# Performance work log

Measured on AMD Instinct MI355X. Metric: run time of the kernel, lower is better.

## Reference

```python
import jax, jax.numpy as jnp
import numpy as np

N = 50000
E = 800000
DIN = 128
DOUT = 128
T = 4  # number of edge types: onset, consecutive, during, rest


def setup_inputs() -> dict:
    key = jax.random.key(0)
    ks = jax.random.split(key, 12)
    s = 1.0 / np.sqrt(DIN)
    inp = {
        "x": jax.random.normal(ks[0], (N, DIN), dtype=jnp.float32),
        "edge_index": jax.random.randint(ks[1], (2, E), 0, N, dtype=jnp.int32),
        "edge_type": jax.random.randint(ks[2], (E,), 0, T, dtype=jnp.int32),
        # stacked per-etype parameters of ResGatedGraphConv
        "Wk": jax.random.uniform(ks[3], (T, DIN, DOUT), jnp.float32, -s, s),
        "bk": jax.random.uniform(ks[4], (T, DOUT), jnp.float32, -s, s),
        "Wq": jax.random.uniform(ks[5], (T, DIN, DOUT), jnp.float32, -s, s),
        "bq": jax.random.uniform(ks[6], (T, DOUT), jnp.float32, -s, s),
        "Wv": jax.random.uniform(ks[7], (T, DIN, DOUT), jnp.float32, -s, s),
        "bv": jax.random.uniform(ks[8], (T, DOUT), jnp.float32, -s, s),
        "Ws": jax.random.uniform(ks[9], (T, DIN, DOUT), jnp.float32, -s, s),
        "b": jax.random.uniform(ks[10], (T, DOUT), jnp.float32, -s, s),
    }
    return inp


def reference(x, edge_index, edge_type, Wk, bk, Wq, bq, Wv, bv, Ws, b):
    # PyG ResGatedGraphConv per edge type t, with edges masked to that type:
    #   out_i = sum_{j->i, type==t} sigmoid(k_i + q_j) * v_j + Ws_t x_i + b_t
    # followed by mean over edge types ('mean' reduction).
    src = edge_index[0]  # j (message source)
    dst = edge_index[1]  # i (message target)
    n = x.shape[0]
    outs = []
    for t in range(T):
        k = x @ Wk[t] + bk[t]  # [N, DOUT]
        q = x @ Wq[t] + bq[t]
        v = x @ Wv[t] + bv[t]
        eta = jax.nn.sigmoid(k[dst] + q[src])        # [E, DOUT]
        msg = eta * v[src]                            # [E, DOUT]
        msg = jnp.where((edge_type == t)[:, None], msg, 0.0)
        agg = jax.ops.segment_sum(msg, dst, num_segments=n)
        outs.append(agg + x @ Ws[t] + b[t])
    return jnp.mean(jnp.stack(outs, axis=0), axis=0)  # [N, DOUT]
```

## Files before the change

kernel.cpp:

```cpp
#include <hip/hip_runtime.h>

typedef unsigned short u16;
typedef unsigned int u32;
typedef __attribute__((ext_vector_type(8))) short bf16x8;
typedef __attribute__((ext_vector_type(4))) float f32x4;
typedef __attribute__((ext_vector_type(4))) u16 u16x4;
typedef __attribute__((ext_vector_type(2))) u32 u32x2;

#define DIM 128
#define ROWB 2304
#define QV_SPAN 384
#define K_OFF 1536
#define S_OFF 2048
#define AS1C(p) ((const __attribute__((address_space(1))) void*)(p))
#define AS3P(p) ((__attribute__((address_space(3))) void*)(p))

#define QKSCALE -1.44269504088896341f

#if defined(__has_builtin)
#if __has_builtin(__builtin_amdgcn_exp2f)
#define EXP2(x) __builtin_amdgcn_exp2f(x)
#endif
#endif
#ifndef EXP2
extern "C" __device__ float __ocml_exp2_f32(float);
#define EXP2(x) __ocml_exp2_f32(x)
#endif

__device__ __forceinline__ u32 f2bf(float f){
  u32 x = __float_as_uint(f);
  return (x + 0x7fffu + ((x >> 16) & 1u)) >> 16;
}
__device__ __forceinline__ float bf2f(u16 u){
  return __uint_as_float(((u32)u) << 16);
}

__global__ __launch_bounds__(256) void prep_kernel(
    const float* __restrict__ x, u16* __restrict__ xb,
    const int* __restrict__ dst, int* __restrict__ cnt, int* __restrict__ rank,
    const float* __restrict__ Wk, const float* __restrict__ bk,
    const float* __restrict__ Wq, const float* __restrict__ bq,
    const float* __restrict__ Wv, const float* __restrict__ bv,
    const float* __restrict__ Ws, const float* __restrict__ bb,
    u16* __restrict__ WcatT, float* __restrict__ biascat,
    int T, int N, int E, int rows){
  int id = blockIdx.x * 256 + threadIdx.x;
  if (id < E){
    rank[id] = atomicAdd(&cnt[dst[id]], 1);
    return;
  }
  id -= E;
  int total_w = (3 * T + 1) * DIM * DIM;
  if (id < total_w){
    int kk = id & (DIM - 1);
    int c  = id >> 7;
    int nt = c >> 7;
    int j  = c & (DIM - 1);
    float wv, bvv;
    if (nt < T)        { wv = Wq[(nt*DIM + kk)*DIM + j] * QKSCALE;       bvv = bq[nt*DIM + j] * QKSCALE; }
    else if (nt < 2*T) { wv = Wv[((nt-T)*DIM + kk)*DIM + j];             bvv = bv[(nt-T)*DIM + j]; }
    else if (nt < 3*T) { wv = Wk[((nt-2*T)*DIM + kk)*DIM + j] * QKSCALE; bvv = bk[(nt-2*T)*DIM + j] * QKSCALE; }
    else {
      float s = 0.f, sb = 0.f;
      for (int t = 0; t < T; ++t){ s += Ws[(t*DIM + kk)*DIM + j]; sb += bb[t*DIM + j]; }
      wv = s / (float)T; bvv = sb / (float)T;
    }
    WcatT[(size_t)c * DIM + kk] = (u16)f2bf(wv);
    if (kk == 0) biascat[c] = bvv;
    return;
  }
  id -= total_w;
  int total_cast = rows * (DIM / 4);
  if (id < total_cast){
    int el = id * 4;
    int node = el >> 7;
    u32x2 pk;
    if (node < N){
      f32x4 v = *(const f32x4*)(x + el);
      pk.x = f2bf(v.x) | (f2bf(v.y) << 16);
      pk.y = f2bf(v.z) | (f2bf(v.w) << 16);
    } else { pk.x = 0u; pk.y = 0u; }
    *(u32x2*)(xb + el) = pk;
  }
}

__global__ __launch_bounds__(256) void scan1_kernel(const int* __restrict__ cnt,
                                                    int* __restrict__ offs,
                                                    int* __restrict__ bsum, int n){
  __shared__ int wsum[4];
  const int tid = threadIdx.x;
  const int lane = tid & 63, wave = tid >> 6;
  const int base = blockIdx.x * 2048 + tid * 8;
  int v[8]; int tot = 0;
#pragma unroll
  for (int j = 0; j < 8; ++j){
    int idx = base + j;
    int val = (idx < n) ? cnt[idx] : 0;
    v[j] = val; tot += val;
  }
  int incl = tot;
#pragma unroll
  for (int d = 1; d < 64; d <<= 1){
    int u = __shfl_up(incl, d, 64);
    if (lane >= d) incl += u;
  }
  if (lane == 63) wsum[wave] = incl;
  __syncthreads();
  int wbase = 0;
#pragma unroll
  for (int w = 0; w < 4; ++w) if (w < wave) wbase += wsum[w];
  int excl = wbase + incl - tot;
  if (tid == 255) bsum[blockIdx.x] = wbase + incl;
#pragma unroll
  for (int j = 0; j < 8; ++j){
    int idx = base + j;
    if (idx < n) offs[idx] = excl;
    excl += v[j];
  }
}

__global__ __launch_bounds__(64) void scan2_kernel(const int* __restrict__ bsum,
                                                   int* __restrict__ boffs, int nb){
  int lane = threadIdx.x;
  int v = (lane < nb) ? bsum[lane] : 0;
  int incl = v;
#pragma unroll
  for (int d = 1; d < 64; d <<= 1){
    int u = __shfl_up(incl, d, 64);
    if (lane >= d) incl += u;
  }
  if (lane < nb) boffs[lane] = incl - v;
}

__global__ __launch_bounds__(256, 4) void gemm_scatter_kernel(
    const u16* __restrict__ xb, const u16* __restrict__ WcatT,
    const float* __restrict__ biascat, char* __restrict__ Y,
    const int* __restrict__ src, const int* __restrict__ dst,
    const int* __restrict__ et, const int* __restrict__ offs,
    const int* __restrict__ boffs, const int* __restrict__ rank,
    int* __restrict__ packed,
    int N, int E, int T, int NB, int mtiles, int nsc){
  __shared__ u16 wt[DIM * DIM];
  int bid = blockIdx.x;
  if (bid < nsc){
    int e = bid * 256 + threadIdx.x;
    if (e < E){
      int d = dst[e];
      int pos = offs[d] + boffs[d >> 11] + rank[e];
      int t = et[e] & 3;
      packed[pos] = src[e] * ROWB + t * QV_SPAN + (t << 28);
    }
    return;
  }
  bid -= nsc;
  int body = NB * (mtiles & ~7);
  int mt, nt;
  if (bid < body){
    int g = bid >> 3, r = bid & 7;
    int a = g / NB;
    mt = a * 8 + r;
    nt = g - a * NB;
  } else {
    int z = bid - body;
    mt = (mtiles & ~7) + z / NB;
    nt = z % NB;
  }
  const int m0 = mt * 128;
  const int n0 = nt * 128;
  const int tid  = threadIdx.x;
  const int wave = tid >> 6;
  const int lane = tid & 63;
  const int l15  = lane & 15;
  const int quad = lane >> 4;
  const int wrow = wave * 32;

  const u16* xrow0 = xb + (size_t)(m0 + wrow + l15) * DIM + quad * 8;
  const u16* xrow1 = xrow0 + 16 * DIM;

  bf16x8 bfr[2][4];
#pragma unroll
  for (int ks = 0; ks < 4; ++ks){
    bfr[0][ks] = *(const bf16x8*)(xrow0 + ks * 32);
    bfr[1][ks] = *(const bf16x8*)(xrow1 + ks * 32);
  }

#pragma unroll
  for (int it = 0; it < 8; ++it){
    int s  = it * 256 + tid;
    int r  = s >> 4;
    int p  = s & 15;
    int lb = p ^ (r & 7);
    int lbase = (it * 256 + wave * 64) * 8;
    __builtin_amdgcn_global_load_lds(AS1C(WcatT + (size_t)(n0 + r) * DIM + lb * 8),
                                     AS3P(wt + lbase), 16, 0, 0);
  }
  __syncthreads();

  f32x4 acc[2][8];
#pragma unroll
  for (int m = 0; m < 2; ++m)
#pragma unroll
    for (int f = 0; f < 8; ++f)
      acc[m][f] = (f32x4){0.f, 0.f, 0.f, 0.f};

#pragma unroll
  for (int ks = 0; ks < 4; ++ks){
    const int pb8 = (((ks * 4 + quad) ^ (l15 & 7)) * 8);
#pragma unroll
    for (int f = 0; f < 8; ++f){
      bf16x8 afr = *(const bf16x8*)&wt[(f * 16 + l15) * DIM + pb8];
      acc[0][f] = __builtin_amdgcn_mfma_f32_16x16x32_bf16(afr, bfr[0][ks], acc[0][f], 0, 0, 0);
      acc[1][f] = __builtin_amdgcn_mfma_f32_16x16x32_bf16(afr, bfr[1][ks], acc[1][f], 0, 0, 0);
    }
  }

  __syncthreads();
  char* lds = (char*)wt;
  const bool is_q = (nt < T);
  const bool is_k = (nt >= 2*T) && (nt < 3*T);
  if (is_q || is_k){
    const int boffb = is_q ? (nt * QV_SPAN) : (K_OFF + (nt - 2*T) * 128);
#pragma unroll
    for (int m = 0; m < 2; ++m){
      const int nl = wrow + m * 16 + l15;
#pragma unroll
      for (int f = 0; f < 8; ++f){
        const int feat = f * 16 + quad * 4;
        f32x4 b4 = *(const f32x4*)&biascat[n0 + feat];
        f32x4 v  = acc[m][f];
        u32 w = __builtin_amdgcn_cvt_pk_fp8_f32(v.x + b4.x, v.y + b4.y, 0, false);
        w = __builtin_amdgcn_cvt_pk_fp8_f32(v.z + b4.z, v.w + b4.w, w, true);
        *(u32*)(lds + nl * 128 + (feat ^ ((nl & 7) << 4))) = w;
      }
    }
    __syncthreads();
    const int seg = tid & 7;
    const int nr0 = tid >> 3;
#pragma unroll
    for (int pass = 0; pass < 4; ++pass){
      const int nl = pass * 32 + nr0;
      f32x4 d = *(const f32x4*)(lds + nl * 128 + ((seg ^ (nl & 7)) << 4));
      *(f32x4*)(Y + (size_t)(m0 + nl) * ROWB + boffb + seg * 16) = d;
    }
  } else {
    const int boffb = (nt < 2*T) ? ((nt - T) * QV_SPAN + 128) : S_OFF;
#pragma unroll
    for (int m = 0; m < 2; ++m){
      const int nl = wrow + m * 16 + l15;
#pragma unroll
      for (int f = 0; f < 8; ++f){
        const int feat = f * 16 + quad * 4;
        f32x4 b4 = *(const f32x4*)&biascat[n0 + feat];
        f32x4 v  = acc[m][f];
        u32 lo = f2bf(v.x + b4.x) | (f2bf(v.y + b4.y) << 16);
        u32 hi = f2bf(v.z + b4.z) | (f2bf(v.w + b4.w) << 16);
        u32x2 pk = {lo, hi};
        *(u32x2*)(lds + nl * 256 + ((feat * 2) ^ ((nl & 7) << 4))) = pk;
      }
    }
    __syncthreads();
    const int seg = tid & 15;
    const int nr0 = tid >> 4;
#pragma unroll
    for (int pass = 0; pass < 8; ++pass){
      const int nl = pass * 16 + nr0;
      f32x4 d = *(const f32x4*)(lds + nl * 256 + ((seg ^ (nl & 7)) << 4));
      *(f32x4*)(Y + (size_t)(m0 + nl) * ROWB + boffb + seg * 16) = d;
    }
  }
}

__global__ __launch_bounds__(256) void agg_kernel(const char* __restrict__ Y,
                                                  const int* __restrict__ offs,
                                                  const int* __restrict__ boffs,
                                                  const int* __restrict__ packed,
                                                  float* __restrict__ out,
                                                  int N, int E, float invT){
  __shared__ float klds[8 * 512];
  const int wave = threadIdx.x >> 6;
  const int lane = threadIdx.x & 63;
  const int half = lane >> 5;
  const int l32  = lane & 31;
  const int hh   = wave * 2 + half;
  const int node = blockIdx.x * 8 + hh;
  const bool valid = node < N;
  const int nc = valid ? node : N - 1;

  const char* yr = Y + (size_t)nc * ROWB;
  char* kb = (char*)(klds + hh * 512 + l32 * 4);

#pragma unroll
  for (int t = 0; t < 4; ++t){
    u32 kw = *(const u32*)(yr + K_OFF + t * 128 + l32 * 4);
    f32x4 kt = (f32x4){ __builtin_amdgcn_cvt_f32_fp8(kw, 0), __builtin_amdgcn_cvt_f32_fp8(kw, 1),
                        __builtin_amdgcn_cvt_f32_fp8(kw, 2), __builtin_amdgcn_cvt_f32_fp8(kw, 3) };
    *(f32x4*)(kb + t * 512) = kt;
  }
  u16x4 sw = *(const u16x4*)(yr + S_OFF + l32 * 8);

  int e0 = 0, e1 = 0;
  if (valid){
    e0 = offs[nc] + boffs[nc >> 11];
    e1 = (nc == N - 1) ? E : (offs[nc + 1] + boffs[(nc + 1) >> 11]);
  }

  const u32 qoff_l = (u32)(l32 * 4);
  const u32 voff_l = (u32)(128 + l32 * 8);

  f32x4 acc = {0.f, 0.f, 0.f, 0.f};
  int e = e0;
  for (; e + 8 <= e1; e += 8){
    int p[8];
#pragma unroll
    for (int j = 0; j < 8; ++j) p[j] = packed[e + j];
    u32 qw[8]; u16x4 vw[8]; f32x4 kt[8];
#pragma unroll
    for (int j = 0; j < 8; ++j){
      u32 base = (u32)p[j] & 0x07FFFFFFu;
      qw[j] = *(const u32*)(Y + base + qoff_l);
      vw[j] = *(const u16x4*)(Y + base + voff_l);
      kt[j] = *(const f32x4*)(kb + (((u32)p[j] >> 19) & 0x600u));
    }
#pragma unroll
    for (int j = 0; j < 8; ++j){
      acc.x += bf2f(vw[j].x) * __builtin_amdgcn_rcpf(1.f + EXP2(kt[j].x + __builtin_amdgcn_cvt_f32_fp8(qw[j], 0)));
      acc.y += bf2f(vw[j].y) * __builtin_amdgcn_rcpf(1.f + EXP2(kt[j].y + __builtin_amdgcn_cvt_f32_fp8(qw[j], 1)));
      acc.z += bf2f(vw[j].z) * __builtin_amdgcn_rcpf(1.f + EXP2(kt[j].z + __builtin_amdgcn_cvt_f32_fp8(qw[j], 2)));
      acc.w += bf2f(vw[j].w) * __builtin_amdgcn_rcpf(1.f + EXP2(kt[j].w + __builtin_amdgcn_cvt_f32_fp8(qw[j], 3)));
    }
  }
  for (; e < e1; ++e){
    int p = packed[e];
    u32 base = (u32)p & 0x07FFFFFFu;
    u32 qw = *(const u32*)(Y + base + qoff_l);
    u16x4 vw = *(const u16x4*)(Y + base + voff_l);
    f32x4 kt = *(const f32x4*)(kb + (((u32)p >> 19) & 0x600u));
    acc.x += bf2f(vw.x) * __builtin_amdgcn_rcpf(1.f + EXP2(kt.x + __builtin_amdgcn_cvt_f32_fp8(qw, 0)));
    acc.y += bf2f(vw.y) * __builtin_amdgcn_rcpf(1.f + EXP2(kt.y + __builtin_amdgcn_cvt_f32_fp8(qw, 1)));
    acc.z += bf2f(vw.z) * __builtin_amdgcn_rcpf(1.f + EXP2(kt.z + __builtin_amdgcn_cvt_f32_fp8(qw, 2)));
    acc.w += bf2f(vw.w) * __builtin_amdgcn_rcpf(1.f + EXP2(kt.w + __builtin_amdgcn_cvt_f32_fp8(qw, 3)));
  }
  if (valid){
    f32x4 o = { invT * acc.x + bf2f(sw.x), invT * acc.y + bf2f(sw.y),
                invT * acc.z + bf2f(sw.z), invT * acc.w + bf2f(sw.w) };
    *(f32x4*)&out[(size_t)node * DIM + l32 * 4] = o;
  }
}

extern "C" void kernel_launch(void* const* d_in, const int* in_sizes, int n_in,
                              void* d_out, int out_size, void* d_ws, size_t ws_size,
                              hipStream_t stream){
  const float* x  = (const float*)d_in[0];
  const int*   ei = (const int*)d_in[1];
  const int*   et = (const int*)d_in[2];
  const float* Wk = (const float*)d_in[3];
  const float* bk = (const float*)d_in[4];
  const float* Wq = (const float*)d_in[5];
  const float* bq = (const float*)d_in[6];
  const float* Wv = (const float*)d_in[7];
  const float* bv = (const float*)d_in[8];
  const float* Ws = (const float*)d_in[9];
  const float* bb = (const float*)d_in[10];
  float* out = (float*)d_out;

  const int N = in_sizes[0] / DIM;
  const int E = in_sizes[2];
  const int T = in_sizes[3] / (DIM * DIM);
  const int NB = 3 * T + 1;
  const int ncol = NB * DIM;
  const int mtiles = (N + 127) / 128;
  const int rows = mtiles * 128;
  const int nscan = (N + 2047) / 2048;
  const int nsc = (E + 255) / 256;

  char* ws = (char*)d_ws;
  size_t off = 0;
  auto alloc = [&](size_t bytes) -> char* {
    char* p = ws + off;
    off = (off + bytes + 255) & ~(size_t)255;
    return p;
  };
  u16*   xb      = (u16*)alloc((size_t)rows * DIM * 2);
  u16*   WcatT   = (u16*)alloc((size_t)ncol * DIM * 2);
  float* biascat = (float*)alloc((size_t)ncol * 4);
  char*  Y       = (char*)alloc((size_t)rows * ROWB);
  int*   cnt     = (int*)alloc((size_t)N * 4);
  int*   offs    = (int*)alloc((size_t)N * 4);
  int*   rank    = (int*)alloc((size_t)E * 4);
  int*   packed  = (int*)alloc((size_t)E * 4);
  int*   bsum    = (int*)alloc((size_t)nscan * 4);
  int*   boffs   = (int*)alloc((size_t)nscan * 4);
  (void)ws_size; (void)n_in; (void)out_size;

  const int* srcp = ei;
  const int* dstp = ei + E;

  hipMemsetAsync(cnt, 0, (size_t)N * 4, stream);
  int prep_total = E + NB * DIM * DIM + rows * (DIM / 4);
  prep_kernel<<<(prep_total + 255) / 256, 256, 0, stream>>>(
      x, xb, dstp, cnt, rank, Wk, bk, Wq, bq, Wv, bv, Ws, bb,
      WcatT, biascat, T, N, E, rows);
  scan1_kernel<<<nscan, 256, 0, stream>>>(cnt, offs, bsum, N);
  scan2_kernel<<<1, 64, 0, stream>>>(bsum, boffs, nscan);
  gemm_scatter_kernel<<<nsc + NB * mtiles, 256, 0, stream>>>(
      xb, WcatT, biascat, Y, srcp, dstp, et, offs, boffs, rank, packed,
      N, E, T, NB, mtiles, nsc);
  agg_kernel<<<(N + 7) / 8, 256, 0, stream>>>(Y, offs, boffs, packed, out, N, E, 1.0f / (float)T);
}
```

Measured before the change: 247.9 us.

## Software-pipeline edge index loads and replace scalar tail with masked rounds in aggregation

The aggregation loop now prefetches the next round's eight packed edge indices while gathering and computing the current round, so index latency overlaps with the Y gathers. The scalar remainder loop is replaced by clamped index loads, with out-of-range edges masked by zeroing their V values, so every node runs whole 8-edge rounds. Launch bounds now request 8 blocks per SM to limit register use. The cost is wasted gather and compute on padded edges for nodes with small degree, plus possible register spills under the tighter bound.

```diff
diff --git a/kernel.cpp b/kernel.cpp
--- a/kernel.cpp
+++ b/kernel.cpp
@@ -270,7 +270,7 @@
   }
 }
 
-__global__ __launch_bounds__(256) void agg_kernel(const char* __restrict__ Y,
+__global__ __launch_bounds__(256, 8) void agg_kernel(const char* __restrict__ Y,
                                                   const int* __restrict__ offs,
                                                   const int* __restrict__ boffs,
                                                   const int* __restrict__ packed,
@@ -289,6 +289,12 @@
   const char* yr = Y + (size_t)nc * ROWB;
   char* kb = (char*)(klds + hh * 512 + l32 * 4);
 
+  int e0 = 0, e1 = 0;
+  if (valid){
+    e0 = offs[nc] + boffs[nc >> 11];
+    e1 = (nc == N - 1) ? E : (offs[nc + 1] + boffs[(nc + 1) >> 11]);
+  }
+
 #pragma unroll
   for (int t = 0; t < 4; ++t){
     u32 kw = *(const u32*)(yr + K_OFF + t * 128 + l32 * 4);
@@ -298,47 +304,52 @@
   }
   u16x4 sw = *(const u16x4*)(yr + S_OFF + l32 * 8);
 
-  int e0 = 0, e1 = 0;
-  if (valid){
-    e0 = offs[nc] + boffs[nc >> 11];
-    e1 = (nc == N - 1) ? E : (offs[nc + 1] + boffs[(nc + 1) >> 11]);
-  }
-
   const u32 qoff_l = (u32)(l32 * 4);
   const u32 voff_l = (u32)(128 + l32 * 8);
 
+  const int nrounds = (e1 - e0 + 7) >> 3;
+  const int last = (e1 > e0) ? (e1 - 1) : 0;
+
   f32x4 acc = {0.f, 0.f, 0.f, 0.f};
+  int pcur[8];
+#pragma unroll
+  for (int j = 0; j < 8; ++j){
+    int idx = e0 + j; idx = idx > last ? last : idx;
+    pcur[j] = packed[idx];
+  }
   int e = e0;
-  for (; e + 8 <= e1; e += 8){
-    int p[8];
-#pragma unroll
-    for (int j = 0; j < 8; ++j) p[j] = packed[e + j];
-    u32 qw[8]; u16x4 vw[8]; f32x4 kt[8];
+  for (int r = 0; r < nrounds; ++r){
+    u32 qw[8]; u16x4 vw[8];
 #pragma unroll
     for (int j = 0; j < 8; ++j){
-      u32 base = (u32)p[j] & 0x07FFFFFFu;
+      u32 base = (u32)pcur[j] & 0x07FFFFFFu;
       qw[j] = *(const u32*)(Y + base + qoff_l);
       vw[j] = *(const u16x4*)(Y + base + voff_l);
-      kt[j] = *(const f32x4*)(kb + (((u32)p[j] >> 19) & 0x600u));
-    }
+    }
+    const int en = e + 8;
+    int pnext[8];
 #pragma unroll
     for (int j = 0; j < 8; ++j){
-      acc.x += bf2f(vw[j].x) * __builtin_amdgcn_rcpf(1.f + EXP2(kt[j].x + __builtin_amdgcn_cvt_f32_fp8(qw[j], 0)));
-      acc.y += bf2f(vw[j].y) * __builtin_amdgcn_rcpf(1.f + EXP2(kt[j].y + __builtin_amdgcn_cvt_f32_fp8(qw[j], 1)));
-      acc.z += bf2f(vw[j].z) * __builtin_amdgcn_rcpf(1.f + EXP2(kt[j].z + __builtin_amdgcn_cvt_f32_fp8(qw[j], 2)));
-      acc.w += bf2f(vw[j].w) * __builtin_amdgcn_rcpf(1.f + EXP2(kt[j].w + __builtin_amdgcn_cvt_f32_fp8(qw[j], 3)));
-    }
-  }
-  for (; e < e1; ++e){
-    int p = packed[e];
-    u32 base = (u32)p & 0x07FFFFFFu;
-    u32 qw = *(const u32*)(Y + base + qoff_l);
-    u16x4 vw = *(const u16x4*)(Y + base + voff_l);
-    f32x4 kt = *(const f32x4*)(kb + (((u32)p >> 19) & 0x600u));
-    acc.x += bf2f(vw.x) * __builtin_amdgcn_rcpf(1.f + EXP2(kt.x + __builtin_amdgcn_cvt_f32_fp8(qw, 0)));
-    acc.y += bf2f(vw.y) * __builtin_amdgcn_rcpf(1.f + EXP2(kt.y + __builtin_amdgcn_cvt_f32_fp8(qw, 1)));
-    acc.z += bf2f(vw.z) * __builtin_amdgcn_rcpf(1.f + EXP2(kt.z + __builtin_amdgcn_cvt_f32_fp8(qw, 2)));
-    acc.w += bf2f(vw.w) * __builtin_amdgcn_rcpf(1.f + EXP2(kt.w + __builtin_amdgcn_cvt_f32_fp8(qw, 3)));
+      int idx = en + j; idx = idx > last ? last : idx;
+      pnext[j] = packed[idx];
+    }
+#pragma unroll
+    for (int j = 0; j < 8; ++j){
+      f32x4 kt = *(const f32x4*)(kb + (((u32)pcur[j] >> 19) & 0x600u));
+      const bool live = (e + j) < e1;
+      u32x2 vv = *(u32x2*)&vw[j];
+      vv.x = live ? vv.x : 0u;
+      vv.y = live ? vv.y : 0u;
+      u16 v0 = (u16)(vv.x & 0xffffu), v1 = (u16)(vv.x >> 16);
+      u16 v2 = (u16)(vv.y & 0xffffu), v3 = (u16)(vv.y >> 16);
+      acc.x += bf2f(v0) * __builtin_amdgcn_rcpf(1.f + EXP2(kt.x + __builtin_amdgcn_cvt_f32_fp8(qw[j], 0)));
+      acc.y += bf2f(v1) * __builtin_amdgcn_rcpf(1.f + EXP2(kt.y + __builtin_amdgcn_cvt_f32_fp8(qw[j], 1)));
+      acc.z += bf2f(v2) * __builtin_amdgcn_rcpf(1.f + EXP2(kt.z + __builtin_amdgcn_cvt_f32_fp8(qw[j], 2)));
+      acc.w += bf2f(v3) * __builtin_amdgcn_rcpf(1.f + EXP2(kt.w + __builtin_amdgcn_cvt_f32_fp8(qw[j], 3)));
+    }
+#pragma unroll
+    for (int j = 0; j < 8; ++j) pcur[j] = pnext[j];
+    e = en;
   }
   if (valid){
     f32x4 o = { invT * acc.x + bf2f(sw.x), invT * acc.y + bf2f(sw.y),
```

Measured after the change: 304.2 us. 1.23x slower.

## Use one wave per node in aggregation with double-buffered edge gathers

Applied to the files above, without the earlier changes.

The aggregation kernel now assigns a full 64-lane wave to each destination node, with each lane handling 2 channels instead of 4, so there are twice as many waves. The edge loop is restructured into blocks of 6 edges with two register buffers, so the gathers for the next block are issued before the current block is computed, which is meant to hide gather latency. Out-of-range indices are clamped and their contributions masked, which adds some wasted loads on the tail. Gathers are narrower per lane, and the total work per node is spread across more threads.

```diff
diff --git a/kernel.cpp b/kernel.cpp
--- a/kernel.cpp
+++ b/kernel.cpp
@@ -4,6 +4,7 @@
 typedef unsigned int u32;
 typedef __attribute__((ext_vector_type(8))) short bf16x8;
 typedef __attribute__((ext_vector_type(4))) float f32x4;
+typedef __attribute__((ext_vector_type(2))) float f32x2;
 typedef __attribute__((ext_vector_type(4))) u16 u16x4;
 typedef __attribute__((ext_vector_type(2))) u32 u32x2;
 
@@ -276,74 +277,89 @@
                                                   const int* __restrict__ packed,
                                                   float* __restrict__ out,
                                                   int N, int E, float invT){
-  __shared__ float klds[8 * 512];
+  __shared__ float klds[4 * 4 * 128];
   const int wave = threadIdx.x >> 6;
   const int lane = threadIdx.x & 63;
-  const int half = lane >> 5;
-  const int l32  = lane & 31;
-  const int hh   = wave * 2 + half;
-  const int node = blockIdx.x * 8 + hh;
+  const int node = blockIdx.x * 4 + wave;
   const bool valid = node < N;
   const int nc = valid ? node : N - 1;
 
   const char* yr = Y + (size_t)nc * ROWB;
-  char* kb = (char*)(klds + hh * 512 + l32 * 4);
-
+
+  float* kwp = klds + wave * 512 + lane * 2;
 #pragma unroll
   for (int t = 0; t < 4; ++t){
-    u32 kw = *(const u32*)(yr + K_OFF + t * 128 + l32 * 4);
-    f32x4 kt = (f32x4){ __builtin_amdgcn_cvt_f32_fp8(kw, 0), __builtin_amdgcn_cvt_f32_fp8(kw, 1),
-                        __builtin_amdgcn_cvt_f32_fp8(kw, 2), __builtin_amdgcn_cvt_f32_fp8(kw, 3) };
-    *(f32x4*)(kb + t * 512) = kt;
-  }
-  u16x4 sw = *(const u16x4*)(yr + S_OFF + l32 * 8);
+    u32 kw = *(const u16*)(yr + K_OFF + t * 128 + lane * 2);
+    f32x2 kt2 = (f32x2){ __builtin_amdgcn_cvt_f32_fp8(kw, 0),
+                         __builtin_amdgcn_cvt_f32_fp8(kw, 1) };
+    *(f32x2*)(kwp + t * 128) = kt2;
+  }
+  u32 sw = *(const u32*)(yr + S_OFF + lane * 4);
 
   int e0 = 0, e1 = 0;
   if (valid){
     e0 = offs[nc] + boffs[nc >> 11];
     e1 = (nc == N - 1) ? E : (offs[nc + 1] + boffs[(nc + 1) >> 11]);
   }
-
-  const u32 qoff_l = (u32)(l32 * 4);
-  const u32 voff_l = (u32)(128 + l32 * 8);
-
-  f32x4 acc = {0.f, 0.f, 0.f, 0.f};
-  int e = e0;
-  for (; e + 8 <= e1; e += 8){
-    int p[8];
-#pragma unroll
-    for (int j = 0; j < 8; ++j) p[j] = packed[e + j];
-    u32 qw[8]; u16x4 vw[8]; f32x4 kt[8];
-#pragma unroll
-    for (int j = 0; j < 8; ++j){
-      u32 base = (u32)p[j] & 0x07FFFFFFu;
-      qw[j] = *(const u32*)(Y + base + qoff_l);
-      vw[j] = *(const u16x4*)(Y + base + voff_l);
-      kt[j] = *(const f32x4*)(kb + (((u32)p[j] >> 19) & 0x600u));
-    }
-#pragma unroll
-    for (int j = 0; j < 8; ++j){
-      acc.x += bf2f(vw[j].x) * __builtin_amdgcn_rcpf(1.f + EXP2(kt[j].x + __builtin_amdgcn_cvt_f32_fp8(qw[j], 0)));
-      acc.y += bf2f(vw[j].y) * __builtin_amdgcn_rcpf(1.f + EXP2(kt[j].y + __builtin_amdgcn_cvt_f32_fp8(qw[j], 1)));
-      acc.z += bf2f(vw[j].z) * __builtin_amdgcn_rcpf(1.f + EXP2(kt[j].z + __builtin_amdgcn_cvt_f32_fp8(qw[j], 2)));
-      acc.w += bf2f(vw[j].w) * __builtin_amdgcn_rcpf(1.f + EXP2(kt[j].w + __builtin_amdgcn_cvt_f32_fp8(qw[j], 3)));
-    }
-  }
-  for (; e < e1; ++e){
-    int p = packed[e];
-    u32 base = (u32)p & 0x07FFFFFFu;
-    u32 qw = *(const u32*)(Y + base + qoff_l);
-    u16x4 vw = *(const u16x4*)(Y + base + voff_l);
-    f32x4 kt = *(const f32x4*)(kb + (((u32)p >> 19) & 0x600u));
-    acc.x += bf2f(vw.x) * __builtin_amdgcn_rcpf(1.f + EXP2(kt.x + __builtin_amdgcn_cvt_f32_fp8(qw, 0)));
-    acc.y += bf2f(vw.y) * __builtin_amdgcn_rcpf(1.f + EXP2(kt.y + __builtin_amdgcn_cvt_f32_fp8(qw, 1)));
-    acc.z += bf2f(vw.z) * __builtin_amdgcn_rcpf(1.f + EXP2(kt.z + __builtin_amdgcn_cvt_f32_fp8(qw, 2)));
-    acc.w += bf2f(vw.w) * __builtin_amdgcn_rcpf(1.f + EXP2(kt.w + __builtin_amdgcn_cvt_f32_fp8(qw, 3)));
+  const int Elast = E - 1;
+  const u32 ql = (u32)(lane << 1);
+  const u32 vl = (u32)(128 + (lane << 2));
+  const char* kbase = (const char*)klds + wave * 2048 + (lane << 3);
+
+  float a0 = 0.f, a1 = 0.f;
+  const int d = e1 - e0;
+  if (d > 0){
+    const int nb = (d + 5) / 6;
+    u32 pA[6], vA[6], pB[6], vB[6];
+    u32 qA[6], qB[6];
+
+#define LOADI(P, Q, V, BI) do {                                        \
+      int _eb = e0 + (BI) * 6;                                         \
+      _Pragma("unroll")                                                \
+      for (int j = 0; j < 6; ++j){                                     \
+        int idx = _eb + j; idx = idx > Elast ? Elast : idx;            \
+        P[j] = (u32)packed[idx];                                       \
+      }                                                                \
+      _Pragma("unroll")                                                \
+      for (int j = 0; j < 6; ++j){                                     \
+        u32 b = P[j] & 0x07FFFFFFu;                                    \
+        Q[j] = (u32)(*(const u16*)(Y + b + ql));                       \
+        V[j] = *(const u32*)(Y + b + vl);                              \
+      }                                                                \
+    } while(0)
+
+#define COMP(P, Q, V, BI) do {                                         \
+      int _eb = e0 + (BI) * 6;                                         \
+      _Pragma("unroll")                                                \
+      for (int j = 0; j < 6; ++j){                                     \
+        f32x2 kt = *(const f32x2*)(kbase + ((P[j] >> 19) & 0x600u));   \
+        u32 vv = (_eb + j < e1) ? V[j] : 0u;                           \
+        float g0 = __builtin_amdgcn_rcpf(1.f + EXP2(kt.x + __builtin_amdgcn_cvt_f32_fp8(Q[j], 0))); \
+        float g1 = __builtin_amdgcn_rcpf(1.f + EXP2(kt.y + __builtin_amdgcn_cvt_f32_fp8(Q[j], 1))); \
+        a0 += bf2f((u16)(vv & 0xffffu)) * g0;                          \
+        a1 += bf2f((u16)(vv >> 16)) * g1;                              \
+      }                                                                \
+    } while(0)
+
+    LOADI(pA, qA, vA, 0);
+    if (nb > 1) LOADI(pB, qB, vB, 1);
+    int bi = 0;
+    while (true){
+      COMP(pA, qA, vA, bi);
+      if (bi + 2 < nb) LOADI(pA, qA, vA, bi + 2);
+      if (bi + 1 >= nb) break;
+      COMP(pB, qB, vB, bi + 1);
+      if (bi + 3 < nb) LOADI(pB, qB, vB, bi + 3);
+      bi += 2;
+      if (bi >= nb) break;
+    }
+#undef LOADI
+#undef COMP
   }
   if (valid){
-    f32x4 o = { invT * acc.x + bf2f(sw.x), invT * acc.y + bf2f(sw.y),
-                invT * acc.z + bf2f(sw.z), invT * acc.w + bf2f(sw.w) };
-    *(f32x4*)&out[(size_t)node * DIM + l32 * 4] = o;
+    f32x2 o = { invT * a0 + bf2f((u16)(sw & 0xffffu)),
+                invT * a1 + bf2f((u16)(sw >> 16)) };
+    *(f32x2*)&out[(size_t)node * DIM + lane * 2] = o;
   }
 }
 
@@ -405,5 +421,5 @@
   gemm_scatter_kernel<<<nsc + NB * mtiles, 256, 0, stream>>>(
       xb, WcatT, biascat, Y, srcp, dstp, et, offs, boffs, rank, packed,
       N, E, T, NB, mtiles, nsc);
-  agg_kernel<<<(N + 7) / 8, 256, 0, stream>>>(Y, offs, boffs, packed, out, N, E, 1.0f / (float)T);
-}
+  agg_kernel<<<(N + 3) / 4, 256, 0, stream>>>(Y, offs, boffs, packed, out, N, E, 1.0f / (float)T);
+}
```

Result: slower. 253.1 us (+2.1%).
